# Kernel tuning notes

Measured on AMD Instinct MI355X. Metric: run time of the kernel, lower is better.

## Reference

```python
import jax, jax.numpy as jnp
import numpy as np

TOP_K = 2
TEMPERATURE = 2.0


def setup_inputs() -> dict:
    key = jax.random.key(0)
    k1, k2, k3 = jax.random.split(key, 3)
    x = jax.random.normal(k1, (16384, 2048), dtype=jnp.float32)
    gate_w = jax.random.normal(k2, (64, 2048), dtype=jnp.float32) * 0.02
    gate_b = jax.random.normal(k3, (64,), dtype=jnp.float32) * 0.02
    expert_maturity = jnp.ones((64,), dtype=jnp.int32)  # all mature -> top-k branch
    return {"x": x, "gate_w": gate_w, "gate_b": gate_b, "expert_maturity": expert_maturity}


def _routing(logits, expert_maturity):
    # branch 1: any immature expert -> temperature softmax over all experts
    def soft_branch(lg):
        return jax.nn.softmax(lg / TEMPERATURE, axis=-1)

    # branch 2: all mature -> top-k selection, softmax over selected, scatter into zeros
    def topk_branch(lg):
        top_w, top_idx = jax.lax.top_k(lg, TOP_K)          # [N, K]
        top_sm = jax.nn.softmax(top_w, axis=-1)            # [N, K]
        n = lg.shape[0]
        rows = jnp.arange(n)[:, None]                      # [N, 1]
        return jnp.zeros_like(lg).at[rows, top_idx].set(top_sm)

    any_immature = jnp.any(expert_maturity == 0)
    return jax.lax.cond(any_immature, soft_branch, topk_branch, logits)


def reference(x, gate_w, gate_b, expert_maturity):
    # logits = x @ W^T + b : [N, E]
    logits = jnp.einsum("nd,ed->ne", x, gate_w) + gate_b
    return _routing(logits, expert_maturity)
```

## Files before the change

### kernel.cpp

```cpp
#include <hip/hip_runtime.h>
#include <math.h>


#define NROWS 16384
#define DIM   2048
#define NEXP  64
#define BM    64
#define TPB   256
#define CH    4
#define NCH   (DIM / 32 / CH)
#define BUFB  32768

typedef __attribute__((ext_vector_type(4))) float f32x4;
typedef __attribute__((ext_vector_type(8))) short bf16x8;

#define MFMA __builtin_amdgcn_mfma_f32_16x16x32_bf16

__device__ __forceinline__ void gl_lds16(const void* g, void* l) {
  __builtin_amdgcn_global_load_lds(
      (const __attribute__((address_space(1))) unsigned char*)g,
      (__attribute__((address_space(3))) unsigned char*)l, 16, 0, 0);
}

__global__ void wfrag_kernel(const float* __restrict__ gw,
                             unsigned short* __restrict__ wsH,
                             unsigned short* __restrict__ wsL) {
  int slot  = blockIdx.x * 64 + threadIdx.x;
  int lane  = slot & 63;
  int t     = (slot >> 6) & 3;
  int kstep = slot >> 8;
  int e  = 16 * t + (lane & 15);
  int k0 = kstep * 32 + (lane >> 4) * 8;
  const float* src = gw + (size_t)e * DIM + k0;
  bf16x8 vh, vl;
#pragma unroll
  for (int j = 0; j < 8; ++j) {
    float w = src[j];
    unsigned u = __float_as_uint(w);
    vh[j] = (short)(u >> 16);
    float hi = __uint_as_float(u & 0xffff0000u);
    float rl = w - hi;
    vl[j] = (short)(__float_as_uint(rl) >> 16);
  }
  ((bf16x8*)wsH)[slot] = vh;
  ((bf16x8*)wsL)[slot] = vl;
}

__global__ __launch_bounds__(TPB, 1)
void router_mfma(const float* __restrict__ x,
                 const unsigned short* __restrict__ wsH,
                 const unsigned short* __restrict__ wsL,
                 const float* __restrict__ gb,
                 const int* __restrict__ mat,
                 float* __restrict__ out) {
  __shared__ __align__(16) char lds[2 * BUFB];
  __shared__ float p_a[BM], p_b[BM];
  __shared__ int   p_i[BM], p_j[BM];
  __shared__ int   s_flag;

  const int tid  = threadIdx.x;
  const int wave = tid >> 6;
  const int lane = tid & 63;
  const int m    = lane & 15;
  const int kg   = lane >> 4;
  const int row0 = blockIdx.x * BM;

  if (tid < 64) {
    unsigned long long b = __ballot(mat[lane] == 0);
    if (lane == 0) s_flag = (b != 0ull) ? 1 : 0;
  }

  f32x4 acc[4];
#pragma unroll
  for (int t = 0; t < 4; ++t) acc[t] = (f32x4)0.0f;

  const unsigned char* wsHb = (const unsigned char*)wsH;
  const unsigned char* wsLb = (const unsigned char*)wsL;
  const float* xb = x + (size_t)(row0 + 16 * wave + m) * DIM + kg * 8;

  auto stageB = [&](int c) {
    const int par = (c & 1) * BUFB;
#pragma unroll
    for (int u = 0; u < 8; ++u) {
      int t = u >> 1, h = u & 1;
      size_t slot = (size_t)((c * CH + wave) * 4 + t);
      gl_lds16((h ? wsLb : wsHb) + slot * 1024 + (size_t)lane * 16,
               lds + par + (wave * 8 + u) * 1024);
    }
  };
  auto loadX = [&](int c, float4 (&dst)[CH][2]) {
    const float* xp = xb + c * (CH * 32);
#pragma unroll
    for (int st = 0; st < CH; ++st) {
      dst[st][0] = *(const float4*)(xp + st * 32);
      dst[st][1] = *(const float4*)(xp + st * 32 + 4);
    }
  };
  auto computeC = [&](int c, float4 (&cur)[CH][2]) {
    const int par = (c & 1) * BUFB;
#pragma unroll
    for (int st = 0; st < CH; ++st) {
      const char* bb = lds + par + st * 8192 + lane * 16;
      bf16x8 bh[4], bl[4];
#pragma unroll
      for (int t = 0; t < 4; ++t) {
        bh[t] = *(const bf16x8*)(bb + (2 * t) * 1024);
        bl[t] = *(const bf16x8*)(bb + (2 * t + 1) * 1024);
      }
      bf16x8 ah, al;
#pragma unroll
      for (int q = 0; q < 2; ++q) {
        float4 v = cur[st][q];
        float ff[4] = {v.x, v.y, v.z, v.w};
#pragma unroll
        for (int j = 0; j < 4; ++j) {
          unsigned u = __float_as_uint(ff[j]);
          ah[q * 4 + j] = (short)(u >> 16);
          float hi = __uint_as_float(u & 0xffff0000u);
          float rl = ff[j] - hi;
          al[q * 4 + j] = (short)(__float_as_uint(rl) >> 16);
        }
      }
#pragma unroll
      for (int t = 0; t < 4; ++t) {
        acc[t] = MFMA(ah, bh[t], acc[t], 0, 0, 0);
        acc[t] = MFMA(ah, bl[t], acc[t], 0, 0, 0);
        acc[t] = MFMA(al, bh[t], acc[t], 0, 0, 0);
      }
    }
  };

  float4 xA[CH][2], xB[CH][2];

  stageB(0);
  __builtin_amdgcn_sched_barrier(0);
  loadX(0, xA);
  asm volatile("s_waitcnt vmcnt(8)" ::: "memory");
  __builtin_amdgcn_sched_barrier(0);
  __builtin_amdgcn_s_barrier();
  __builtin_amdgcn_sched_barrier(0);

  auto body = [&](int c, float4 (&cur)[CH][2], float4 (&nxt)[CH][2]) {
    const bool more = (c + 1 < NCH);
    if (more) {
      stageB(c + 1);
      __builtin_amdgcn_sched_barrier(0);
      loadX(c + 1, nxt);
    }
    computeC(c, cur);
    if (more) {
      asm volatile("s_waitcnt vmcnt(8)" ::: "memory");
      __builtin_amdgcn_sched_barrier(0);
      __builtin_amdgcn_s_barrier();
      __builtin_amdgcn_sched_barrier(0);
    }
  };

#pragma unroll 1
  for (int c = 0; c < NCH; c += 2) {
    body(c, xA, xB);
    body(c + 1, xB, xA);
  }

  float* slab = (float*)lds;
  {
    float gbv[4];
#pragma unroll
    for (int t = 0; t < 4; ++t) gbv[t] = gb[16 * t + m];
#pragma unroll
    for (int t = 0; t < 4; ++t)
#pragma unroll
      for (int reg = 0; reg < 4; ++reg)
        slab[(16 * wave + kg * 4 + reg) * NEXP + 16 * t + m] = acc[t][reg] + gbv[t];
  }
  __syncthreads();

  const int flag = s_flag;

  if (tid < BM) {
    const float* rowp = slab + tid * NEXP;
    if (flag == 0) {
      float m1 = -1e30f, m2 = -1e30f;
      int i1 = 0, i2 = 0;
      for (int ee = 0; ee < NEXP; ++ee) {
        int e = (ee + tid) & (NEXP - 1);
        float v = rowp[e];
        if (v > m1) { m2 = m1; i2 = i1; m1 = v; i1 = e; }
        else if (v > m2) { m2 = v; i2 = e; }
      }
      float t = expf(m2 - m1);
      float pa = 1.0f / (1.0f + t);
      p_a[tid] = pa;
      p_b[tid] = t * pa;
      p_i[tid] = i1;
      p_j[tid] = i2;
    } else {
      float mx = -1e30f;
      for (int ee = 0; ee < NEXP; ++ee)
        mx = fmaxf(mx, rowp[(ee + tid) & (NEXP - 1)]);
      float ssum = 0.0f;
      for (int ee = 0; ee < NEXP; ++ee)
        ssum += expf((rowp[(ee + tid) & (NEXP - 1)] - mx) * 0.5f);
      p_a[tid] = mx;
      p_b[tid] = 1.0f / ssum;
    }
  }
  __syncthreads();

#pragma unroll
  for (int i = 0; i < 4; ++i) {
    int q  = tid + i * TPB;
    int r  = q >> 4;
    int e0 = (q & 15) * 4;
    float4 v;
    if (flag == 0) {
      int i1 = p_i[r], i2 = p_j[r];
      float a = p_a[r], b = p_b[r];
      v.x = (e0 + 0 == i1) ? a : (e0 + 0 == i2) ? b : 0.0f;
      v.y = (e0 + 1 == i1) ? a : (e0 + 1 == i2) ? b : 0.0f;
      v.z = (e0 + 2 == i1) ? a : (e0 + 2 == i2) ? b : 0.0f;
      v.w = (e0 + 3 == i1) ? a : (e0 + 3 == i2) ? b : 0.0f;
    } else {
      float mx = p_a[r], inv = p_b[r];
      const float* rowp = slab + r * NEXP + e0;
      v.x = expf((rowp[0] - mx) * 0.5f) * inv;
      v.y = expf((rowp[1] - mx) * 0.5f) * inv;
      v.z = expf((rowp[2] - mx) * 0.5f) * inv;
      v.w = expf((rowp[3] - mx) * 0.5f) * inv;
    }
    *(float4*)(out + (size_t)(row0 + r) * NEXP + e0) = v;
  }
}

extern "C" void kernel_launch(void* const* d_in, const int* in_sizes, int n_in,
                              void* d_out, int out_size, void* d_ws, size_t ws_size,
                              hipStream_t stream) {
  const float* x  = (const float*)d_in[0];
  const float* gw = (const float*)d_in[1];
  const float* gb = (const float*)d_in[2];
  const int*   mt = (const int*)d_in[3];
  float* outp = (float*)d_out;
  (void)in_sizes; (void)n_in; (void)out_size; (void)ws_size;

  unsigned short* wsH = (unsigned short*)d_ws;
  unsigned short* wsL = wsH + 64 * DIM;

  wfrag_kernel<<<256, 64, 0, stream>>>(gw, wsH, wsL);
  router_mfma<<<NROWS / BM, TPB, 0, stream>>>(x, wsH, wsL, gb, mt, outp);
}
```

Before: 214.2 us.

## Load weight fragments directly from global into registers, drop LDS staging

Replaces the double-buffered LDS staging of bf16 weight fragments (global_load_lds plus block barriers) with direct per-wave register loads from global memory/L2, software-pipelined one k-step ahead. X loads become nontemporal and are prefetched two k-steps ahead. This removes the LDS traffic and the workgroup barriers, at the cost of each wave fetching the full weight stream itself from cache and a shallower prefetch depth.

```diff
diff --git a/kernel.cpp b/kernel.cpp
--- a/kernel.cpp
+++ b/kernel.cpp
@@ -7,20 +7,12 @@
 #define NEXP  64
 #define BM    64
 #define TPB   256
-#define CH    4
-#define NCH   (DIM / 32 / CH)
-#define BUFB  32768
+#define NK    (DIM / 32)
 
 typedef __attribute__((ext_vector_type(4))) float f32x4;
 typedef __attribute__((ext_vector_type(8))) short bf16x8;
 
 #define MFMA __builtin_amdgcn_mfma_f32_16x16x32_bf16
-
-__device__ __forceinline__ void gl_lds16(const void* g, void* l) {
-  __builtin_amdgcn_global_load_lds(
-      (const __attribute__((address_space(1))) unsigned char*)g,
-      (__attribute__((address_space(3))) unsigned char*)l, 16, 0, 0);
-}
 
 __global__ void wfrag_kernel(const float* __restrict__ gw,
                              unsigned short* __restrict__ wsH,
@@ -53,7 +45,7 @@
                  const float* __restrict__ gb,
                  const int* __restrict__ mat,
                  float* __restrict__ out) {
-  __shared__ __align__(16) char lds[2 * BUFB];
+  __shared__ __align__(16) float slab[BM * NEXP];
   __shared__ float p_a[BM], p_b[BM];
   __shared__ int   p_i[BM], p_j[BM];
   __shared__ int   s_flag;
@@ -74,95 +66,70 @@
 #pragma unroll
   for (int t = 0; t < 4; ++t) acc[t] = (f32x4)0.0f;
 
-  const unsigned char* wsHb = (const unsigned char*)wsH;
-  const unsigned char* wsLb = (const unsigned char*)wsL;
+  const bf16x8* wsHf = (const bf16x8*)wsH;
+  const bf16x8* wsLf = (const bf16x8*)wsL;
   const float* xb = x + (size_t)(row0 + 16 * wave + m) * DIM + kg * 8;
 
-  auto stageB = [&](int c) {
-    const int par = (c & 1) * BUFB;
-#pragma unroll
-    for (int u = 0; u < 8; ++u) {
-      int t = u >> 1, h = u & 1;
-      size_t slot = (size_t)((c * CH + wave) * 4 + t);
-      gl_lds16((h ? wsLb : wsHb) + slot * 1024 + (size_t)lane * 16,
-               lds + par + (wave * 8 + u) * 1024);
-    }
-  };
-  auto loadX = [&](int c, float4 (&dst)[CH][2]) {
-    const float* xp = xb + c * (CH * 32);
-#pragma unroll
-    for (int st = 0; st < CH; ++st) {
-      dst[st][0] = *(const float4*)(xp + st * 32);
-      dst[st][1] = *(const float4*)(xp + st * 32 + 4);
-    }
-  };
-  auto computeC = [&](int c, float4 (&cur)[CH][2]) {
-    const int par = (c & 1) * BUFB;
-#pragma unroll
-    for (int st = 0; st < CH; ++st) {
-      const char* bb = lds + par + st * 8192 + lane * 16;
-      bf16x8 bh[4], bl[4];
-#pragma unroll
-      for (int t = 0; t < 4; ++t) {
-        bh[t] = *(const bf16x8*)(bb + (2 * t) * 1024);
-        bl[t] = *(const bf16x8*)(bb + (2 * t + 1) * 1024);
+  auto loadB = [&](int k, bf16x8 (&dh)[4], bf16x8 (&dl)[4]) {
+#pragma unroll
+    for (int t = 0; t < 4; ++t) {
+      size_t idx = (size_t)(4 * k + t) * 64 + lane;
+      dh[t] = wsHf[idx];
+      dl[t] = wsLf[idx];
+    }
+  };
+  auto loadX = [&](int k, f32x4 (&d)[2]) {
+    const float* xp = xb + k * 32;
+    d[0] = __builtin_nontemporal_load((const f32x4*)xp);
+    d[1] = __builtin_nontemporal_load((const f32x4*)(xp + 4));
+  };
+  auto cvt = [&](const f32x4 (&xv)[2], bf16x8& ah, bf16x8& al) {
+#pragma unroll
+    for (int q = 0; q < 2; ++q)
+#pragma unroll
+      for (int j = 0; j < 4; ++j) {
+        float f = xv[q][j];
+        unsigned u = __float_as_uint(f);
+        ah[q * 4 + j] = (short)(u >> 16);
+        float hi = __uint_as_float(u & 0xffff0000u);
+        al[q * 4 + j] = (short)(__float_as_uint(f - hi) >> 16);
       }
+  };
+  auto mfma12 = [&](const bf16x8& ah, const bf16x8& al,
+                    const bf16x8 (&bh)[4], const bf16x8 (&bl)[4]) {
+#pragma unroll
+    for (int t = 0; t < 4; ++t) {
+      acc[t] = MFMA(ah, bh[t], acc[t], 0, 0, 0);
+      acc[t] = MFMA(ah, bl[t], acc[t], 0, 0, 0);
+      acc[t] = MFMA(al, bh[t], acc[t], 0, 0, 0);
+    }
+  };
+
+  bf16x8 Bh0[4], Bl0[4], Bh1[4], Bl1[4];
+  f32x4  xq0[2], xq1[2];
+
+  loadB(0, Bh0, Bl0);
+  loadX(0, xq0);
+  loadX(1, xq1);
+
+#pragma unroll 1
+  for (int k = 0; k < NK; k += 2) {
+    {
       bf16x8 ah, al;
-#pragma unroll
-      for (int q = 0; q < 2; ++q) {
-        float4 v = cur[st][q];
-        float ff[4] = {v.x, v.y, v.z, v.w};
-#pragma unroll
-        for (int j = 0; j < 4; ++j) {
-          unsigned u = __float_as_uint(ff[j]);
-          ah[q * 4 + j] = (short)(u >> 16);
-          float hi = __uint_as_float(u & 0xffff0000u);
-          float rl = ff[j] - hi;
-          al[q * 4 + j] = (short)(__float_as_uint(rl) >> 16);
-        }
-      }
-#pragma unroll
-      for (int t = 0; t < 4; ++t) {
-        acc[t] = MFMA(ah, bh[t], acc[t], 0, 0, 0);
-        acc[t] = MFMA(ah, bl[t], acc[t], 0, 0, 0);
-        acc[t] = MFMA(al, bh[t], acc[t], 0, 0, 0);
-      }
-    }
-  };
-
-  float4 xA[CH][2], xB[CH][2];
-
-  stageB(0);
-  __builtin_amdgcn_sched_barrier(0);
-  loadX(0, xA);
-  asm volatile("s_waitcnt vmcnt(8)" ::: "memory");
-  __builtin_amdgcn_sched_barrier(0);
-  __builtin_amdgcn_s_barrier();
-  __builtin_amdgcn_sched_barrier(0);
-
-  auto body = [&](int c, float4 (&cur)[CH][2], float4 (&nxt)[CH][2]) {
-    const bool more = (c + 1 < NCH);
-    if (more) {
-      stageB(c + 1);
-      __builtin_amdgcn_sched_barrier(0);
-      loadX(c + 1, nxt);
-    }
-    computeC(c, cur);
-    if (more) {
-      asm volatile("s_waitcnt vmcnt(8)" ::: "memory");
-      __builtin_amdgcn_sched_barrier(0);
-      __builtin_amdgcn_s_barrier();
-      __builtin_amdgcn_sched_barrier(0);
-    }
-  };
-
-#pragma unroll 1
-  for (int c = 0; c < NCH; c += 2) {
-    body(c, xA, xB);
-    body(c + 1, xB, xA);
-  }
-
-  float* slab = (float*)lds;
+      cvt(xq0, ah, al);
+      loadX(k + 2 < NK ? k + 2 : NK - 2, xq0);
+      loadB(k + 1, Bh1, Bl1);
+      mfma12(ah, al, Bh0, Bl0);
+    }
+    {
+      bf16x8 ah, al;
+      cvt(xq1, ah, al);
+      loadX(k + 3 < NK ? k + 3 : NK - 1, xq1);
+      loadB(k + 2 < NK ? k + 2 : NK - 1, Bh0, Bl0);
+      mfma12(ah, al, Bh1, Bl1);
+    }
+  }
+
   {
     float gbv[4];
 #pragma unroll
```

After: 218.0 us. About the same (+1.8%).
